# Optimization experiments

Hardware: AMD Instinct MI355X
Metric: run time of the kernel (lower is better)

The kernel has to match this reference:

```python
import jax, jax.numpy as jnp
import numpy as np

A = 2
IMG_C = 3
IMG_H = 64
IMG_W = 96
N_OBJ = 5   # OBJS + STACKS with REMOVE_BG
B = 64
P = 4       # number of predicate nets
CONV_OUT = 32


def setup_inputs() -> dict:
    key = jax.random.key(0)
    k0, k1, k2, k3 = jax.random.split(key, 4)
    state = jax.random.normal(k0, (B, N_OBJ, IMG_C, IMG_H, IMG_W), jnp.float32)
    state_next = jax.random.normal(k1, (B, N_OBJ, IMG_C, IMG_H, IMG_W), jnp.float32)
    # uniform object count (structural max N=5) so tuple count is static
    n_obj = jnp.full((B,), N_OBJ, dtype=jnp.int32)
    temp = jnp.float32(0.5)
    # stacked params for the P predicate nets (conv + linear head)
    conv_w = jax.random.normal(k2, (P * CONV_OUT, A * IMG_C, 3, 3), jnp.float32) * 0.05
    conv_b = jnp.zeros((P * CONV_OUT,), jnp.float32)
    w2 = jax.random.normal(k3, (P, CONV_OUT), jnp.float32) * 0.1
    b2 = jnp.zeros((P,), jnp.float32)
    return {"state": state, "state_next": state_next, "conv_w": conv_w,
            "conv_b": conv_b, "w2": w2, "b2": b2, "n_obj": n_obj, "temp": temp}


def _build_tuples(s, n):
    # cartesian_prod(arange(n), arange(n)) -> ordered pairs (i, j)
    ii = jnp.repeat(jnp.arange(n), n)   # [n*n]
    jj = jnp.tile(jnp.arange(n), n)     # [n*n]
    a = s[:, ii]                        # [B, n*n, C, H, W]
    b = s[:, jj]
    t = jnp.concatenate([a, b], axis=2)             # [B, n*n, A*C, H, W]
    return t.reshape(-1, A * IMG_C, IMG_H, IMG_W)   # [B*n*n, 6, H, W]


def _predicates(t, conv_w, conv_b, w2, b2, temp):
    # fused conv over all P nets (stacked output channels)
    y = jax.lax.conv_general_dilated(
        t, conv_w, window_strides=(2, 2), padding='SAME',
        dimension_numbers=('NCHW', 'OIHW', 'NCHW'))
    y = jax.nn.relu(y + conv_b[None, :, None, None])
    y = y.mean(axis=(2, 3)).reshape(-1, P, CONV_OUT)   # [T, P, 32]
    logits = jnp.einsum('tpc,pc->tp', y, w2) + b2      # [T, P]
    return jax.nn.sigmoid(logits / temp)


def reference(state, state_next, conv_w, conv_b, w2, b2, n_obj, temp):
    n = N_OBJ  # uniform ragged case: all n_obj entries equal the max
    tuples = _build_tuples(state, n)
    tuples_next = _build_tuples(state_next, n)
    preds = _predicates(tuples, conv_w, conv_b, w2, b2, temp)
    preds_next = _predicates(tuples_next, conv_w, conv_b, w2, b2, temp)
    # adjacency: column per tuple, one-hot in the owning sample's row
    T = B * n * n
    adj = (jnp.arange(T)[None, :] // (n * n) == jnp.arange(B)[:, None]).astype(jnp.float32)
    return preds, preds_next, adj
```

## Files before the change

### kernel.cpp

```cpp
#include <hip/hip_runtime.h>
#include <math.h>

#define BQ 64
#define NOBJ 5
#define CIN 3
#define IMG_H 64
#define IMG_W 96
#define OH 32
#define OW 48
#define NPAIR 25
#define PP 4
#define CONV_OUT 32

#define NRG 16
#define NPOS 96
#define XK 32
#define X_U32 (NOBJ * NPOS * XK / 2)
#define X_UNITS (NOBJ * NPOS * 4)

#define NPRED (2 * 1600 * PP)
#define ADJ_N (BQ * 1600)

typedef __fp16   h2 __attribute__((ext_vector_type(2)));
typedef _Float16 half8 __attribute__((ext_vector_type(8)));
typedef float    float4_ __attribute__((ext_vector_type(4)));
typedef float    float2_ __attribute__((ext_vector_type(2)));
typedef unsigned int uint4_ __attribute__((ext_vector_type(4)));

__global__ __launch_bounds__(512) void conv_pair_mfma(
    const float* __restrict__ state,
    const float* __restrict__ state_next,
    const float* __restrict__ conv_w,
    const float* __restrict__ conv_b,
    const float* __restrict__ w2,
    float* __restrict__ T,
    float* __restrict__ out)
{
    __shared__ __align__(16) unsigned int sX32[X_U32];

    const int tid = threadIdx.x;
    const int rg  = blockIdx.x;
    const int b   = blockIdx.y;
    const int src = blockIdx.z;

    const float* g = (src == 0 ? state : state_next)
                   + (size_t)b * NOBJ * CIN * IMG_H * IMG_W;
    const int R0 = rg * 4;

    if (src == 1 && tid < 100) {
        int a  = (rg + NRG * b) * 100 + tid;
        int bb = a / 1600;
        int t  = a - bb * 1600;
        out[NPRED + a] = (t / NPAIR == bb) ? 1.0f : 0.0f;
    }

    const int wave = tid >> 6;
    const int lane = tid & 63;
    const int quad = lane >> 4;
    const int ocl  = lane & 15;

    const int mt  = wave;
    const int p   = mt >> 1;
    const int row = mt * 16 + ocl;

    half8 wa, wb;
    #pragma unroll
    for (int j = 0; j < 8; ++j) {
        int k = quad * 8 + j;
        float va = 0.f, vb = 0.f;
        if (k < 27) {
            va = conv_w[row * 54 + k];
            vb = conv_w[row * 54 + 27 + k];
        } else if (k == 27) {
            va = conv_b[row];
        }
        wa[j] = (_Float16)va;
        wb[j] = (_Float16)vb;
    }
    h2 w2h01, w2h23;
    {
        const float* wp = w2 + p * CONV_OUT + (mt & 1) * 16 + quad * 4;
        w2h01 = __builtin_amdgcn_cvt_pkrtz(wp[0], wp[1]);
        w2h23 = __builtin_amdgcn_cvt_pkrtz(wp[2], wp[3]);
    }

    {
        const int subk = tid & 3;
        int koff[8], khv[8], kwv[8];
        float padf[8];
        bool kval[8];
        #pragma unroll
        for (int j = 0; j < 8; ++j) {
            int k = subk * 8 + j;
            if (k < 27) {
                int ci = k / 9;
                int r9 = k - ci * 9;
                int kh = r9 / 3;
                int kw = r9 - kh * 3;
                koff[j] = ci * (IMG_H * IMG_W) + kh * IMG_W + kw;
                khv[j] = kh; kwv[j] = kw; kval[j] = true; padf[j] = 0.f;
            } else {
                koff[j] = 0; khv[j] = 0; kwv[j] = 0; kval[j] = false;
                padf[j] = (k == 27) ? 1.0f : 0.f;
            }
        }
        for (int u = tid; u < X_UNITS; u += 512) {
            int pl  = (u >> 2) % NPOS;
            int obj = u / (NPOS * 4);
            int rl  = (pl >= 48) ? 1 : 0;
            int pc  = pl - rl * 48;
            int gr0 = R0 + 2 * rl;
            int gc0 = 2 * pc;
            const float* gp = g + obj * (CIN * IMG_H * IMG_W) + gr0 * IMG_W + gc0;
            float fv[8];
            #pragma unroll
            for (int j = 0; j < 8; ++j) {
                float v = padf[j];
                if (kval[j] && (gr0 + khv[j] < IMG_H) && (gc0 + kwv[j] < IMG_W))
                    v = gp[koff[j]];
                fv[j] = v;
            }
            uint4_ w4;
            w4.x = __builtin_bit_cast(unsigned int, __builtin_amdgcn_cvt_pkrtz(fv[0], fv[1]));
            w4.y = __builtin_bit_cast(unsigned int, __builtin_amdgcn_cvt_pkrtz(fv[2], fv[3]));
            w4.z = __builtin_bit_cast(unsigned int, __builtin_amdgcn_cvt_pkrtz(fv[4], fv[5]));
            w4.w = __builtin_bit_cast(unsigned int, __builtin_amdgcn_cvt_pkrtz(fv[6], fv[7]));
            int swk = subk ^ ((pl >> 1) & 3);
            *(uint4_*)&sX32[(size_t)(obj * (NPOS * 16) + pl * 16 + swk * 4)] = w4;
        }
    }

    __syncthreads();

    const float4_ zero4 = {0.f, 0.f, 0.f, 0.f};
    const h2 hz = {(__fp16)0.f, (__fp16)0.f};

    float acc[NPAIR];
    #pragma unroll
    for (int q = 0; q < NPAIR; ++q) acc[q] = 0.f;

    #pragma unroll
    for (int nt = 0; nt < 6; ++nt) {
        const int rl  = nt / 3;
        const int c0  = (nt - rl * 3) * 16;
        const int pos = rl * 48 + c0 + ocl;
        const int sw  = (pos >> 1) & 3;
        const int sbase = pos * 16 + ((quad ^ sw) << 2);

        half8 xf[NOBJ];
        h2 ah01[NOBJ], ah23[NOBJ];
        #pragma unroll
        for (int obj = 0; obj < NOBJ; ++obj) {
            xf[obj] = *(const half8*)&sX32[sbase + obj * (NPOS * 16)];
            float4_ a = __builtin_amdgcn_mfma_f32_16x16x32_f16(wa, xf[obj], zero4, 0, 0, 0);
            ah01[obj] = __builtin_amdgcn_cvt_pkrtz(a[0], a[1]);
            ah23[obj] = __builtin_amdgcn_cvt_pkrtz(a[2], a[3]);
        }

        #pragma unroll
        for (int jo = 0; jo < NOBJ; ++jo) {
            float4_ bq = __builtin_amdgcn_mfma_f32_16x16x32_f16(wb, xf[jo], zero4, 0, 0, 0);
            h2 bh01 = __builtin_amdgcn_cvt_pkrtz(bq[0], bq[1]);
            h2 bh23 = __builtin_amdgcn_cvt_pkrtz(bq[2], bq[3]);
            #pragma unroll
            for (int i = 0; i < NOBJ; ++i) {
                h2 s0 = ah01[i] + bh01;
                h2 s1 = ah23[i] + bh23;
                s0 = __builtin_elementwise_max(s0, hz);
                s1 = __builtin_elementwise_max(s1, hz);
                float t0 = __builtin_amdgcn_fdot2(s0, w2h01, acc[i * NOBJ + jo], false);
                acc[i * NOBJ + jo] = __builtin_amdgcn_fdot2(s1, w2h23, t0, false);
            }
        }
    }

    float myv = 0.f;
    #pragma unroll
    for (int q = 0; q < NPAIR; ++q) {
        float rr = acc[q];
        #pragma unroll
        for (int off = 32; off > 0; off >>= 1)
            rr += __shfl_xor(rr, off, 64);
        if (lane == q) myv = rr;
    }
    if (lane < NPAIR)
        T[((((size_t)src * BQ + b) * NRG + rg) * NPAIR + lane) * 8 + mt] = myv;
}

__global__ __launch_bounds__(256) void pred_kernel(
    const float* __restrict__ T,
    const float* __restrict__ b2,
    const float* __restrict__ temp,
    float* __restrict__ out)
{
    int gid = blockIdx.x * blockDim.x + threadIdx.x;
    int idx = gid >> 2;
    int h   = gid & 3;
    if (idx >= NPRED) return;
    int p   = idx & 3;
    int t   = (idx >> 2) % 1600;
    int src = idx / 6400;
    int bb  = t / NPAIR;
    int pr  = t - bb * NPAIR;
    const float* base = T + ((((size_t)src * BQ + bb) * NRG) * NPAIR + pr) * 8 + 2 * p;
    float sum = 0.f;
    #pragma unroll
    for (int r = 0; r < 4; ++r) {
        int rgi = h * 4 + r;
        float2_ v = *(const float2_*)&base[(size_t)rgi * NPAIR * 8];
        sum += v[0] + v[1];
    }
    sum += __shfl_xor(sum, 1, 64);
    sum += __shfl_xor(sum, 2, 64);
    if (h == 0) {
        float logit = sum * (1.0f / (OH * OW)) + b2[p];
        float x = logit / temp[0];
        out[idx] = 1.0f / (1.0f + expf(-x));
    }
}

extern "C" void kernel_launch(void* const* d_in, const int* in_sizes, int n_in,
                              void* d_out, int out_size, void* d_ws, size_t ws_size,
                              hipStream_t stream)
{
    const float* state      = (const float*)d_in[0];
    const float* state_next = (const float*)d_in[1];
    const float* conv_w     = (const float*)d_in[2];
    const float* conv_b     = (const float*)d_in[3];
    const float* w2         = (const float*)d_in[4];
    const float* b2         = (const float*)d_in[5];
    const float* temp       = (const float*)d_in[7];

    float* out = (float*)d_out;
    float* T   = (float*)d_ws;

    dim3 grid1(NRG, BQ, 2);
    conv_pair_mfma<<<grid1, 512, 0, stream>>>(state, state_next, conv_w, conv_b,
                                              w2, T, out);

    pred_kernel<<<(NPRED * 4 + 255) / 256, 256, 0, stream>>>(T, b2, temp, out);
}
```

Measured before the change: 152.3 us.

## Stage im2col tile one output row at a time to halve shared memory

The shared-memory im2col tile now holds one output row (48 positions) instead of two, and the staging plus MFMA compute loop runs twice per block with a barrier between passes. The aim is to halve LDS use per block (about 30KB down to about 15KB) so more 512-thread blocks fit per CU and global loads overlap compute across blocks. In exchange it adds a second __syncthreads, and global loads and compute are serialised within each block.

```diff
diff --git a/kernel.cpp b/kernel.cpp
--- a/kernel.cpp
+++ b/kernel.cpp
@@ -13,10 +13,10 @@
 #define CONV_OUT 32
 
 #define NRG 16
-#define NPOS 96
+#define ROWPOS 48
 #define XK 32
-#define X_U32 (NOBJ * NPOS * XK / 2)
-#define X_UNITS (NOBJ * NPOS * 4)
+#define X_U32 (NOBJ * ROWPOS * XK / 2)
+#define X_UNITS (NOBJ * ROWPOS * 4)
 
 #define NPRED (2 * 1600 * PP)
 #define ADJ_N (BQ * 1600)
@@ -84,53 +84,25 @@
         w2h23 = __builtin_amdgcn_cvt_pkrtz(wp[2], wp[3]);
     }
 
-    {
-        const int subk = tid & 3;
-        int koff[8], khv[8], kwv[8];
-        float padf[8];
-        bool kval[8];
-        #pragma unroll
-        for (int j = 0; j < 8; ++j) {
-            int k = subk * 8 + j;
-            if (k < 27) {
-                int ci = k / 9;
-                int r9 = k - ci * 9;
-                int kh = r9 / 3;
-                int kw = r9 - kh * 3;
-                koff[j] = ci * (IMG_H * IMG_W) + kh * IMG_W + kw;
-                khv[j] = kh; kwv[j] = kw; kval[j] = true; padf[j] = 0.f;
-            } else {
-                koff[j] = 0; khv[j] = 0; kwv[j] = 0; kval[j] = false;
-                padf[j] = (k == 27) ? 1.0f : 0.f;
-            }
-        }
-        for (int u = tid; u < X_UNITS; u += 512) {
-            int pl  = (u >> 2) % NPOS;
-            int obj = u / (NPOS * 4);
-            int rl  = (pl >= 48) ? 1 : 0;
-            int pc  = pl - rl * 48;
-            int gr0 = R0 + 2 * rl;
-            int gc0 = 2 * pc;
-            const float* gp = g + obj * (CIN * IMG_H * IMG_W) + gr0 * IMG_W + gc0;
-            float fv[8];
-            #pragma unroll
-            for (int j = 0; j < 8; ++j) {
-                float v = padf[j];
-                if (kval[j] && (gr0 + khv[j] < IMG_H) && (gc0 + kwv[j] < IMG_W))
-                    v = gp[koff[j]];
-                fv[j] = v;
-            }
-            uint4_ w4;
-            w4.x = __builtin_bit_cast(unsigned int, __builtin_amdgcn_cvt_pkrtz(fv[0], fv[1]));
-            w4.y = __builtin_bit_cast(unsigned int, __builtin_amdgcn_cvt_pkrtz(fv[2], fv[3]));
-            w4.z = __builtin_bit_cast(unsigned int, __builtin_amdgcn_cvt_pkrtz(fv[4], fv[5]));
-            w4.w = __builtin_bit_cast(unsigned int, __builtin_amdgcn_cvt_pkrtz(fv[6], fv[7]));
-            int swk = subk ^ ((pl >> 1) & 3);
-            *(uint4_*)&sX32[(size_t)(obj * (NPOS * 16) + pl * 16 + swk * 4)] = w4;
-        }
-    }
-
-    __syncthreads();
+    const int subk = tid & 3;
+    int koff[8], khv[8], kwv[8];
+    float padf[8];
+    bool kval[8];
+    #pragma unroll
+    for (int j = 0; j < 8; ++j) {
+        int k = subk * 8 + j;
+        if (k < 27) {
+            int ci = k / 9;
+            int r9 = k - ci * 9;
+            int kh = r9 / 3;
+            int kw = r9 - kh * 3;
+            koff[j] = ci * (IMG_H * IMG_W) + kh * IMG_W + kw;
+            khv[j] = kh; kwv[j] = kw; kval[j] = true; padf[j] = 0.f;
+        } else {
+            koff[j] = 0; khv[j] = 0; kwv[j] = 0; kval[j] = false;
+            padf[j] = (k == 27) ? 1.0f : 0.f;
+        }
+    }
 
     const float4_ zero4 = {0.f, 0.f, 0.f, 0.f};
     const h2 hz = {(__fp16)0.f, (__fp16)0.f};
@@ -140,36 +112,66 @@
     for (int q = 0; q < NPAIR; ++q) acc[q] = 0.f;
 
     #pragma unroll
-    for (int nt = 0; nt < 6; ++nt) {
-        const int rl  = nt / 3;
-        const int c0  = (nt - rl * 3) * 16;
-        const int pos = rl * 48 + c0 + ocl;
-        const int sw  = (pos >> 1) & 3;
-        const int sbase = pos * 16 + ((quad ^ sw) << 2);
-
-        half8 xf[NOBJ];
-        h2 ah01[NOBJ], ah23[NOBJ];
+    for (int rlp = 0; rlp < 2; ++rlp) {
+        if (rlp) __syncthreads();
+
+        {
+            const int gr0 = R0 + 2 * rlp;
+            for (int u = tid; u < X_UNITS; u += 512) {
+                int pl  = (u >> 2) % ROWPOS;
+                int obj = u / (ROWPOS * 4);
+                int gc0 = 2 * pl;
+                const float* gp = g + obj * (CIN * IMG_H * IMG_W) + gr0 * IMG_W + gc0;
+                float fv[8];
+                #pragma unroll
+                for (int j = 0; j < 8; ++j) {
+                    float v = padf[j];
+                    if (kval[j] && (gr0 + khv[j] < IMG_H) && (gc0 + kwv[j] < IMG_W))
+                        v = gp[koff[j]];
+                    fv[j] = v;
+                }
+                uint4_ w4;
+                w4.x = __builtin_bit_cast(unsigned int, __builtin_amdgcn_cvt_pkrtz(fv[0], fv[1]));
+                w4.y = __builtin_bit_cast(unsigned int, __builtin_amdgcn_cvt_pkrtz(fv[2], fv[3]));
+                w4.z = __builtin_bit_cast(unsigned int, __builtin_amdgcn_cvt_pkrtz(fv[4], fv[5]));
+                w4.w = __builtin_bit_cast(unsigned int, __builtin_amdgcn_cvt_pkrtz(fv[6], fv[7]));
+                int swk = subk ^ ((pl >> 1) & 3);
+                *(uint4_*)&sX32[(size_t)(obj * (ROWPOS * 16) + pl * 16 + swk * 4)] = w4;
+            }
+        }
+
+        __syncthreads();
+
         #pragma unroll
-        for (int obj = 0; obj < NOBJ; ++obj) {
-            xf[obj] = *(const half8*)&sX32[sbase + obj * (NPOS * 16)];
-            float4_ a = __builtin_amdgcn_mfma_f32_16x16x32_f16(wa, xf[obj], zero4, 0, 0, 0);
-            ah01[obj] = __builtin_amdgcn_cvt_pkrtz(a[0], a[1]);
-            ah23[obj] = __builtin_amdgcn_cvt_pkrtz(a[2], a[3]);
-        }
-
-        #pragma unroll
-        for (int jo = 0; jo < NOBJ; ++jo) {
-            float4_ bq = __builtin_amdgcn_mfma_f32_16x16x32_f16(wb, xf[jo], zero4, 0, 0, 0);
-            h2 bh01 = __builtin_amdgcn_cvt_pkrtz(bq[0], bq[1]);
-            h2 bh23 = __builtin_amdgcn_cvt_pkrtz(bq[2], bq[3]);
+        for (int nt3 = 0; nt3 < 3; ++nt3) {
+            const int pos = nt3 * 16 + ocl;
+            const int sw  = (pos >> 1) & 3;
+            const int sbase = pos * 16 + ((quad ^ sw) << 2);
+
+            half8 xf[NOBJ];
+            h2 ah01[NOBJ], ah23[NOBJ];
             #pragma unroll
-            for (int i = 0; i < NOBJ; ++i) {
-                h2 s0 = ah01[i] + bh01;
-                h2 s1 = ah23[i] + bh23;
-                s0 = __builtin_elementwise_max(s0, hz);
-                s1 = __builtin_elementwise_max(s1, hz);
-                float t0 = __builtin_amdgcn_fdot2(s0, w2h01, acc[i * NOBJ + jo], false);
-                acc[i * NOBJ + jo] = __builtin_amdgcn_fdot2(s1, w2h23, t0, false);
+            for (int obj = 0; obj < NOBJ; ++obj) {
+                xf[obj] = *(const half8*)&sX32[sbase + obj * (ROWPOS * 16)];
+                float4_ a = __builtin_amdgcn_mfma_f32_16x16x32_f16(wa, xf[obj], zero4, 0, 0, 0);
+                ah01[obj] = __builtin_amdgcn_cvt_pkrtz(a[0], a[1]);
+                ah23[obj] = __builtin_amdgcn_cvt_pkrtz(a[2], a[3]);
+            }
+
+            #pragma unroll
+            for (int jo = 0; jo < NOBJ; ++jo) {
+                float4_ bq = __builtin_amdgcn_mfma_f32_16x16x32_f16(wb, xf[jo], zero4, 0, 0, 0);
+                h2 bh01 = __builtin_amdgcn_cvt_pkrtz(bq[0], bq[1]);
+                h2 bh23 = __builtin_amdgcn_cvt_pkrtz(bq[2], bq[3]);
+                #pragma unroll
+                for (int i = 0; i < NOBJ; ++i) {
+                    h2 s0 = ah01[i] + bh01;
+                    h2 s1 = ah23[i] + bh23;
+                    s0 = __builtin_elementwise_max(s0, hz);
+                    s1 = __builtin_elementwise_max(s1, hz);
+                    float t0 = __builtin_amdgcn_fdot2(s0, w2h01, acc[i * NOBJ + jo], false);
+                    acc[i * NOBJ + jo] = __builtin_amdgcn_fdot2(s1, w2h23, t0, false);
+                }
             }
         }
     }
```

New measurement: 158.6 us. 1.04x slower.
